# Optimization experiments

Measured on AMD Instinct MI355X. Metric: run time of the kernel, lower is better.

## Reference

```python
import jax, jax.numpy as jnp
import numpy as np

N = 20000      # nodes
E = 160000     # edges
IN = 32        # in_dim == hidden_dim
H = 32         # hidden_dim
EF = 95        # edge_feat_dim
EH = 64        # edge_hidden
G = 64         # graphs in batch
EPS = 1e-5     # BatchNorm eps


def setup_inputs() -> dict:
    key = jax.random.key(0)
    ks = jax.random.split(key, 40)
    d = {}
    d["x"] = jax.random.normal(ks[0], (N, IN), dtype=jnp.float32)
    d["edge_src"] = jax.random.randint(ks[1], (E,), 0, N)
    d["edge_dst"] = jax.random.randint(ks[2], (E,), 0, N)
    d["edge_attr"] = jax.random.normal(ks[3], (E, EF), dtype=jnp.float32)
    d["batch"] = jnp.sort(jax.random.randint(ks[4], (N,), 0, G))
    k = 5
    for i, c_in in enumerate([IN, H]):
        c_out = H
        d[f"conv{i}_W1"] = jax.random.normal(ks[k], (EF, EH)) * 0.1; k += 1
        d[f"conv{i}_b1"] = jnp.zeros((EH,), jnp.float32)
        d[f"conv{i}_W2"] = jax.random.normal(ks[k], (EH, c_in * c_out)) * 0.02; k += 1
        d[f"conv{i}_b2"] = jnp.zeros((c_in * c_out,), jnp.float32)
        d[f"conv{i}_root"] = jax.random.normal(ks[k], (c_in, c_out)) * 0.1; k += 1
        d[f"conv{i}_bias"] = jnp.zeros((c_out,), jnp.float32)
        d[f"bn{i}_g"] = jnp.ones((c_out,), jnp.float32)
        d[f"bn{i}_b"] = jnp.zeros((c_out,), jnp.float32)
        d[f"bn{i}_rm"] = jnp.zeros((c_out,), jnp.float32)
        d[f"bn{i}_rv"] = jnp.ones((c_out,), jnp.float32)
    d["lin1_W"] = jax.random.normal(ks[k], (H, H)) * 0.1; k += 1
    d["lin1_b"] = jnp.zeros((H,), jnp.float32)
    d["lin2_W"] = jax.random.normal(ks[k], (H, 2)) * 0.1; k += 1
    d["lin2_b"] = jnp.zeros((2,), jnp.float32)
    return d


def _nnconv(x, src, dst, e, W1, b1, W2, b2, root, bias, c_in, c_out):
    # edge MLP -> per-edge weight matrix Theta: [E, c_in, c_out]
    h = jax.nn.relu(e @ W1 + b1)
    theta = (h @ W2 + b2).reshape(-1, c_in, c_out)
    # message: x_src (gather) times per-edge matrix, scatter-add to dst
    msg = jnp.einsum('ei,eio->eo', x[src], theta)
    agg = jax.ops.segment_sum(msg, dst, num_segments=N)
    return agg + x @ root + bias


def _bn_eval(x, g, b, rm, rv):
    return (x - rm) * jax.lax.rsqrt(rv + EPS) * g + b


def reference(x, edge_src, edge_dst, edge_attr, batch,
              conv0_W1, conv0_b1, conv0_W2, conv0_b2, conv0_root, conv0_bias,
              bn0_g, bn0_b, bn0_rm, bn0_rv,
              conv1_W1, conv1_b1, conv1_W2, conv1_b2, conv1_root, conv1_bias,
              bn1_g, bn1_b, bn1_rm, bn1_rv,
              lin1_W, lin1_b, lin2_W, lin2_b):
    x = _nnconv(x, edge_src, edge_dst, edge_attr,
                conv0_W1, conv0_b1, conv0_W2, conv0_b2, conv0_root, conv0_bias, IN, H)
    x = jax.nn.relu(_bn_eval(x, bn0_g, bn0_b, bn0_rm, bn0_rv))
    x = _nnconv(x, edge_src, edge_dst, edge_attr,
                conv1_W1, conv1_b1, conv1_W2, conv1_b2, conv1_root, conv1_bias, H, H)
    x = jax.nn.relu(_bn_eval(x, bn1_g, bn1_b, bn1_rm, bn1_rv))
    # global max pool over graphs
    g = jax.ops.segment_max(x, batch, num_segments=G)
    g = jax.nn.relu(g @ lin1_W + lin1_b)
    return g @ lin2_W + lin2_b
```

## Files before the change

kernel.cpp:

```cpp
#include <hip/hip_runtime.h>

#define NN   20000
#define NE   160000
#define HD   32
#define EFD  95
#define EHD  64
#define NG   64
#define EPSF 1e-5f

__global__ __launch_bounds__(256) void zero_kernel(float* __restrict__ p, int n) {
    int i = blockIdx.x * 256 + threadIdx.x;
    if (i < n) p[i] = 0.f;
}

__global__ __launch_bounds__(256) void hist_kernel(const int* __restrict__ idx,
                                                   int* __restrict__ hist) {
    const int e = blockIdx.x * 256 + threadIdx.x;
    atomicAdd(&hist[idx[e]], 1);
}

__global__ __launch_bounds__(1024) void scan_kernel(const int* __restrict__ hist,
                                                    int* __restrict__ rowptr,
                                                    int* __restrict__ cursor) {
    __shared__ int part[1024];
    const int t = threadIdx.x;
    const int base = t * 20;
    int s = 0;
    #pragma unroll
    for (int k = 0; k < 20; ++k) {
        const int idx = base + k;
        if (idx < NN) s += hist[idx];
    }
    part[t] = s;
    __syncthreads();
    for (int off = 1; off < 1024; off <<= 1) {
        int v = 0;
        if (t >= off) v = part[t - off];
        __syncthreads();
        if (t >= off) part[t] += v;
        __syncthreads();
    }
    int run = part[t] - s;
    #pragma unroll
    for (int k = 0; k < 20; ++k) {
        const int idx = base + k;
        if (idx < NN) {
            rowptr[idx] = run;
            cursor[idx] = run;
            run += hist[idx];
        }
    }
    if (t == 0) rowptr[NN] = NE;
}

__global__ __launch_bounds__(256) void scatter_dst_kernel(const int* __restrict__ dst,
                                                          int* __restrict__ cursor,
                                                          int* __restrict__ sortpos) {
    const int e = blockIdx.x * 256 + threadIdx.x;
    sortpos[e] = atomicAdd(&cursor[dst[e]], 1);
}

__global__ __launch_bounds__(256) void scatter_src_kernel(const int* __restrict__ src,
                                                          const int* __restrict__ sortpos_d,
                                                          int* __restrict__ cursor,
                                                          int* __restrict__ ssorted,
                                                          int* __restrict__ wpos,
                                                          int* __restrict__ esorted) {
    const int e = blockIdx.x * 256 + threadIdx.x;
    const int s = src[e];
    const int pos = atomicAdd(&cursor[s], 1);
    ssorted[pos] = s;
    wpos[pos]    = sortpos_d[e];
    esorted[pos] = e;
}

__global__ __launch_bounds__(256) void edge_mlp_kernel(
    const float* __restrict__ ea, const float* __restrict__ W1,
    const float* __restrict__ b1, float* __restrict__ hT)
{
    __shared__ float elds[128 * EFD];
    const int tid = threadIdx.x;
    const int e0  = blockIdx.x * 128;
    const float4* s4 = reinterpret_cast<const float4*>(ea + (size_t)e0 * EFD);
    float4* d4 = reinterpret_cast<float4*>(elds);
    #pragma unroll
    for (int i = 0; i < 12; ++i) {
        const int idx = tid + i * 256;
        if (idx < (128 * EFD / 4)) d4[idx] = s4[idx];
    }
    __syncthreads();
    const int el = tid & 127;
    const int hh = (tid >> 7) * 32;
    const int e  = e0 + el;
    float acc[32];
    #pragma unroll
    for (int k = 0; k < 32; ++k) acc[k] = b1[hh + k];
    const float* er = elds + el * EFD;
    #pragma unroll 5
    for (int j = 0; j < EFD; ++j) {
        const float ej = er[j];
        const float* w1r = W1 + j * EHD + hh;
        #pragma unroll
        for (int k = 0; k < 32; ++k)
            acc[k] = fmaf(ej, w1r[k], acc[k]);
    }
    #pragma unroll
    for (int k = 0; k < 32; ++k)
        hT[(hh + k) * NE + e] = fmaxf(acc[k], 0.f);
}

__global__ __launch_bounds__(256) void edge_mlp_v7_kernel(
    const float* __restrict__ ea,
    const float* __restrict__ W1,
    const float* __restrict__ b1,
    float*       __restrict__ hs)
{
    __shared__ float alds[64 * 100];
    __shared__ float wlds[96 * 64];
    const int tid = threadIdx.x;
    const int e0  = blockIdx.x * 64;

    {
        const float4* s4 = reinterpret_cast<const float4*>(ea + (size_t)e0 * EFD);
        #pragma unroll
        for (int it = 0; it < 6; ++it) {
            const int idx4 = tid + it * 256;
            if (idx4 < (64 * EFD / 4)) {
                const float4 v = s4[idx4];
                const unsigned f = (unsigned)idx4 * 4u;
                const float vv[4] = {v.x, v.y, v.z, v.w};
                #pragma unroll
                for (int t = 0; t < 4; ++t) {
                    const unsigned ft = f + t;
                    const unsigned et = (ft * 44151u) >> 22;
                    const unsigned jt = ft - 95u * et;
                    alds[et * 100 + jt] = vv[t];
                }
            }
        }
    }
    {
        const float4* w4 = reinterpret_cast<const float4*>(W1);
        float4* d4 = reinterpret_cast<float4*>(wlds);
        #pragma unroll
        for (int it = 0; it < 6; ++it) {
            const int idx4 = tid + it * 256;
            if (idx4 < (EFD * EHD / 4)) d4[idx4] = w4[idx4];
        }
    }
    if (tid < 64) {
        alds[tid * 100 + 95] = 0.f;
        wlds[95 * 64 + tid]  = 0.f;
    }
    __syncthreads();

    const int tx = tid & 15;
    const int ty = tid >> 4;

    float acc[4][4];
    {
        const float4 bv4 = *reinterpret_cast<const float4*>(b1 + 4 * tx);
        const float bb[4] = {bv4.x, bv4.y, bv4.z, bv4.w};
        #pragma unroll
        for (int i = 0; i < 4; ++i)
            #pragma unroll
            for (int c = 0; c < 4; ++c)
                acc[i][c] = bb[c];
    }

    for (int jq = 0; jq < 24; ++jq) {
        float w[4][4];
        #pragma unroll
        for (int r = 0; r < 4; ++r) {
            const float4 wv = *reinterpret_cast<const float4*>(
                &wlds[(4 * jq + r) * 64 + 4 * tx]);
            w[r][0] = wv.x; w[r][1] = wv.y; w[r][2] = wv.z; w[r][3] = wv.w;
        }
        #pragma unroll
        for (int i = 0; i < 4; ++i) {
            const float4 av = *reinterpret_cast<const float4*>(
                &alds[(4 * ty + i) * 100 + 4 * jq]);
            #pragma unroll
            for (int c = 0; c < 4; ++c) {
                float t0 = fmaf(av.x, w[0][c], acc[i][c]);
                t0 = fmaf(av.y, w[1][c], t0);
                t0 = fmaf(av.z, w[2][c], t0);
                acc[i][c] = fmaf(av.w, w[3][c], t0);
            }
        }
    }

    #pragma unroll
    for (int i = 0; i < 4; ++i) {
        const int e = e0 + 4 * ty + i;
        float4 v;
        v.x = fmaxf(acc[i][0], 0.f);
        v.y = fmaxf(acc[i][1], 0.f);
        v.z = fmaxf(acc[i][2], 0.f);
        v.w = fmaxf(acc[i][3], 0.f);
        *reinterpret_cast<float4*>(hs + (size_t)e * EHD + 4 * tx) = v;
    }
}

__global__ __launch_bounds__(256) void tmat_kernel(
    const float* __restrict__ xin,
    const float* __restrict__ W2,
    float*       __restrict__ T)
{
    const int nb = blockIdx.x * 8;
    const int c  = blockIdx.y * 256 + threadIdx.x;
    const int kh = c >> 5, o = c & 31;

    float w[32];
    const float* wp = W2 + kh * 1024 + o;
    #pragma unroll
    for (int i = 0; i < 32; ++i) w[i] = wp[i * 32];

    #pragma unroll
    for (int nj = 0; nj < 8; ++nj) {
        const float* xr = xin + (nb + nj) * HD;
        float a0 = 0.f, a1 = 0.f;
        #pragma unroll
        for (int i = 0; i < 32; i += 2) {
            a0 = fmaf(xr[i],     w[i],     a0);
            a1 = fmaf(xr[i + 1], w[i + 1], a1);
        }
        T[(size_t)(nb + nj) * 2048 + c] = a0 + a1;
    }
}

__global__ __launch_bounds__(256) void bvec_kernel(
    const float* __restrict__ xin, const float* __restrict__ b2,
    float* __restrict__ bv)
{
    const int gid = blockIdx.x * 256 + threadIdx.x;
    const int n = gid >> 5, o = gid & 31;
    const float* xr = xin + n * HD;
    float a = 0.f;
    #pragma unroll
    for (int i = 0; i < 32; ++i)
        a = fmaf(xr[i], b2[i * HD + o], a);
    bv[gid] = a;
}

__global__ __launch_bounds__(256) void emsg_kernel(
    const int*   __restrict__ ssorted, const int* __restrict__ wpos,
    const int*   __restrict__ esorted,
    const float* __restrict__ hs,
    const float* __restrict__ T,
    const float* __restrict__ bv,
    float*       __restrict__ msg)
{
    __shared__ float hl[8 * EHD];
    const int tid = threadIdx.x;
    const int p0  = blockIdx.x * 8;

    if (tid < 128) {
        const int q   = tid >> 4;
        const int eid = esorted[p0 + q];
        reinterpret_cast<float4*>(hl)[tid] =
            reinterpret_cast<const float4*>(hs + (size_t)eid * EHD)[tid & 15];
    }
    __syncthreads();

    const int sl = tid >> 5, o = tid & 31;
    const int p  = p0 + sl;
    const int s  = ssorted[p];
    const int wp = wpos[p];

    float hreg[EHD];
    #pragma unroll
    for (int q = 0; q < 16; ++q) {
        const float4 v = reinterpret_cast<const float4*>(hl + sl * EHD)[q];
        hreg[q * 4] = v.x; hreg[q * 4 + 1] = v.y;
        hreg[q * 4 + 2] = v.z; hreg[q * 4 + 3] = v.w;
    }

    const float* tr = T + (size_t)s * 2048 + o;
    float a0 = bv[s * HD + o], a1 = 0.f;
    #pragma unroll
    for (int kh = 0; kh < EHD; kh += 2) {
        a0 = fmaf(hreg[kh],     tr[kh * 32],       a0);
        a1 = fmaf(hreg[kh + 1], tr[(kh + 1) * 32], a1);
    }
    msg[(size_t)wp * HD + o] = a0 + a1;
}

__global__ __launch_bounds__(64) void nnconv_kernel(
    const float* __restrict__ xin, const int* __restrict__ src,
    const int* __restrict__ sortpos, const float* __restrict__ hT,
    const float* __restrict__ W2, const float* __restrict__ b2,
    float* __restrict__ msg)
{
    const int e  = blockIdx.x * 64 + threadIdx.x;
    const int oh = blockIdx.y * 16;
    const int s  = src[e];
    const int sp = sortpos[e];
    float xs[HD];
    {
        const float* xr = xin + s * HD;
        #pragma unroll
        for (int i = 0; i < HD; i += 4) {
            const float4 v = *reinterpret_cast<const float4*>(xr + i);
            xs[i] = v.x; xs[i + 1] = v.y; xs[i + 2] = v.z; xs[i + 3] = v.w;
        }
    }
    float acc[16];
    #pragma unroll
    for (int o = 0; o < 16; ++o) acc[o] = 0.f;
    #pragma unroll 1
    for (int kh = 0; kh < EHD; ++kh) {
        const float hk = hT[kh * NE + e];
        const float* w2k = W2 + kh * (HD * HD) + oh;
        #pragma unroll
        for (int i = 0; i < HD; ++i) {
            const float p = hk * xs[i];
            #pragma unroll
            for (int o = 0; o < 16; ++o)
                acc[o] = fmaf(p, w2k[i * HD + o], acc[o]);
        }
    }
    #pragma unroll 1
    for (int i = 0; i < HD; ++i) {
        const float xi = xs[i];
        const float* b2r = b2 + i * HD + oh;
        #pragma unroll
        for (int o = 0; o < 16; ++o)
            acc[o] = fmaf(xi, b2r[o], acc[o]);
    }
    float* mr = msg + sp * HD + oh;
    #pragma unroll
    for (int q = 0; q < 4; ++q) {
        float4 v;
        v.x = acc[q * 4 + 0]; v.y = acc[q * 4 + 1];
        v.z = acc[q * 4 + 2]; v.w = acc[q * 4 + 3];
        *reinterpret_cast<float4*>(mr + q * 4) = v;
    }
}

__global__ __launch_bounds__(256) void node_update_kernel(
    const int*   __restrict__ rowptr, const float* __restrict__ msg,
    const float* __restrict__ xin,
    const float* __restrict__ root, const float* __restrict__ bias,
    const float* __restrict__ bg, const float* __restrict__ bb,
    const float* __restrict__ brm, const float* __restrict__ brv,
    float* __restrict__ xout)
{
    const int gid = blockIdx.x * 256 + threadIdx.x;
    const int n = gid >> 5, o = gid & 31;
    float a = 0.f;
    const int j0 = rowptr[n], j1 = rowptr[n + 1];
    for (int j = j0; j < j1; ++j)
        a += msg[j * HD + o];
    const float* xr = xin + n * HD;
    #pragma unroll
    for (int i = 0; i < HD; ++i)
        a = fmaf(xr[i], root[i * HD + o], a);
    a += bias[o];
    a = (a - brm[o]) * rsqrtf(brv[o] + EPSF) * bg[o] + bb[o];
    xout[gid] = fmaxf(a, 0.f);
}

__global__ __launch_bounds__(256) void node_update_pool_kernel(
    const int*   __restrict__ rowptr, const float* __restrict__ msg,
    const float* __restrict__ xin, const int* __restrict__ batch,
    const float* __restrict__ root, const float* __restrict__ bias,
    const float* __restrict__ bg, const float* __restrict__ bb,
    const float* __restrict__ brm, const float* __restrict__ brv,
    float* __restrict__ g)
{
    const int gid = blockIdx.x * 256 + threadIdx.x;
    const int n = gid >> 5, o = gid & 31;
    float a = 0.f;
    const int j0 = rowptr[n], j1 = rowptr[n + 1];
    for (int j = j0; j < j1; ++j)
        a += msg[j * HD + o];
    const float* xr = xin + n * HD;
    #pragma unroll
    for (int i = 0; i < HD; ++i)
        a = fmaf(xr[i], root[i * HD + o], a);
    a += bias[o];
    a = (a - brm[o]) * rsqrtf(brv[o] + EPSF) * bg[o] + bb[o];
    a = fmaxf(a, 0.f);
    atomicMax(reinterpret_cast<int*>(g) + batch[n] * HD + o, __float_as_int(a));
}

__global__ __launch_bounds__(256) void pool_kernel(
    const float* __restrict__ x, const int* __restrict__ batch,
    float* __restrict__ g)
{
    const int gid = blockIdx.x * 256 + threadIdx.x;
    const int n = gid >> 5, o = gid & 31;
    const float v = x[gid];
    atomicMax(reinterpret_cast<int*>(g) + batch[n] * HD + o, __float_as_int(v));
}

__global__ __launch_bounds__(64) void head_kernel(
    const float* __restrict__ g, const float* __restrict__ l1W,
    const float* __restrict__ l1b, const float* __restrict__ l2W,
    const float* __restrict__ l2b, float* __restrict__ out)
{
    const int gr = threadIdx.x;
    const float* grow = g + gr * HD;
    float hv[HD];
    #pragma unroll
    for (int o = 0; o < HD; ++o) hv[o] = l1b[o];
    #pragma unroll
    for (int i = 0; i < HD; ++i) {
        const float gi = grow[i];
        #pragma unroll
        for (int o = 0; o < HD; ++o)
            hv[o] = fmaf(gi, l1W[i * HD + o], hv[o]);
    }
    float o0 = l2b[0], o1 = l2b[1];
    #pragma unroll
    for (int o = 0; o < HD; ++o) {
        const float r = fmaxf(hv[o], 0.f);
        o0 = fmaf(r, l2W[o * 2 + 0], o0);
        o1 = fmaf(r, l2W[o * 2 + 1], o1);
    }
    out[gr * 2 + 0] = o0;
    out[gr * 2 + 1] = o1;
}

extern "C" void kernel_launch(void* const* d_in, const int* in_sizes, int n_in,
                              void* d_out, int out_size, void* d_ws, size_t ws_size,
                              hipStream_t stream)
{
    const float* x     = (const float*)d_in[0];
    const int*   esrc  = (const int*)  d_in[1];
    const int*   edst  = (const int*)  d_in[2];
    const float* eattr = (const float*)d_in[3];
    const int*   batch = (const int*)  d_in[4];

    const float* c0W1   = (const float*)d_in[5];
    const float* c0b1   = (const float*)d_in[6];
    const float* c0W2   = (const float*)d_in[7];
    const float* c0b2   = (const float*)d_in[8];
    const float* c0root = (const float*)d_in[9];
    const float* c0bias = (const float*)d_in[10];
    const float* bn0g   = (const float*)d_in[11];
    const float* bn0b   = (const float*)d_in[12];
    const float* bn0rm  = (const float*)d_in[13];
    const float* bn0rv  = (const float*)d_in[14];

    const float* c1W1   = (const float*)d_in[15];
    const float* c1b1   = (const float*)d_in[16];
    const float* c1W2   = (const float*)d_in[17];
    const float* c1b2   = (const float*)d_in[18];
    const float* c1root = (const float*)d_in[19];
    const float* c1bias = (const float*)d_in[20];
    const float* bn1g   = (const float*)d_in[21];
    const float* bn1b   = (const float*)d_in[22];
    const float* bn1rm  = (const float*)d_in[23];
    const float* bn1rv  = (const float*)d_in[24];

    const float* l1W = (const float*)d_in[25];
    const float* l1b = (const float*)d_in[26];
    const float* l2W = (const float*)d_in[27];
    const float* l2b = (const float*)d_in[28];

    float* ws   = (float*)d_ws;
    float* hbuf = ws;
    float* msg  = ws + 10240000;
    float* x1   = ws + 15360000;
    float* x2   = ws + 16000000;
    float* gbuf = ws + 16640000;
    int* hist_d    = (int*)(ws + 16642048);
    int* hist_s    = (int*)(ws + 16662048);
    int* rowptr_d  = (int*)(ws + 16682048);
    int* cursor_d  = (int*)(ws + 16702049);
    int* sortpos_d = (int*)(ws + 16722049);
    int* rowptr_s  = (int*)(ws + 16882049);
    int* cursor_s  = (int*)(ws + 16902050);
    int* ssorted   = (int*)(ws + 16922050);
    int* wpos      = (int*)(ws + 17082050);
    int* esorted   = (int*)(ws + 17242050);
    float* bv      = ws + 17402050;
    float* T       = ws + 18042050;
    const size_t NEED_NEW = (size_t)59002050 * 4;
    const bool use_fast = (ws_size >= NEED_NEW);

    zero_kernel<<<165, 256, 0, stream>>>(gbuf, 42048);

    hist_kernel<<<NE / 256, 256, 0, stream>>>(edst, hist_d);
    scan_kernel<<<1, 1024, 0, stream>>>(hist_d, rowptr_d, cursor_d);
    scatter_dst_kernel<<<NE / 256, 256, 0, stream>>>(edst, cursor_d, sortpos_d);

    if (use_fast) {
        hist_kernel<<<NE / 256, 256, 0, stream>>>(esrc, hist_s);
        scan_kernel<<<1, 1024, 0, stream>>>(hist_s, rowptr_s, cursor_s);
        scatter_src_kernel<<<NE / 256, 256, 0, stream>>>(esrc, sortpos_d, cursor_s,
                                                         ssorted, wpos, esorted);
        const dim3 tgrid(NN / 8, 8);
        bvec_kernel<<<NN * HD / 256, 256, 0, stream>>>(x, c0b2, bv);
        tmat_kernel<<<tgrid, 256, 0, stream>>>(x, c0W2, T);
        edge_mlp_v7_kernel<<<NE / 64, 256, 0, stream>>>(eattr, c0W1, c0b1, hbuf);
        emsg_kernel<<<NE / 8, 256, 0, stream>>>(ssorted, wpos, esorted, hbuf, T, bv, msg);
        node_update_kernel<<<NN * HD / 256, 256, 0, stream>>>(rowptr_d, msg, x, c0root, c0bias,
                                                              bn0g, bn0b, bn0rm, bn0rv, x1);
        bvec_kernel<<<NN * HD / 256, 256, 0, stream>>>(x1, c1b2, bv);
        tmat_kernel<<<tgrid, 256, 0, stream>>>(x1, c1W2, T);
        edge_mlp_v7_kernel<<<NE / 64, 256, 0, stream>>>(eattr, c1W1, c1b1, hbuf);
        emsg_kernel<<<NE / 8, 256, 0, stream>>>(ssorted, wpos, esorted, hbuf, T, bv, msg);
        node_update_pool_kernel<<<NN * HD / 256, 256, 0, stream>>>(rowptr_d, msg, x1, batch,
                                                                   c1root, c1bias,
                                                                   bn1g, bn1b, bn1rm, bn1rv, gbuf);
    } else {
        const dim3 egrid64(NE / 64, 2);
        edge_mlp_kernel<<<NE / 128, 256, 0, stream>>>(eattr, c0W1, c0b1, hbuf);
        nnconv_kernel<<<egrid64, 64, 0, stream>>>(x, esrc, sortpos_d, hbuf, c0W2, c0b2, msg);
        node_update_kernel<<<NN * HD / 256, 256, 0, stream>>>(rowptr_d, msg, x, c0root, c0bias,
                                                              bn0g, bn0b, bn0rm, bn0rv, x1);
        edge_mlp_kernel<<<NE / 128, 256, 0, stream>>>(eattr, c1W1, c1b1, hbuf);
        nnconv_kernel<<<egrid64, 64, 0, stream>>>(x1, esrc, sortpos_d, hbuf, c1W2, c1b2, msg);
        node_update_kernel<<<NN * HD / 256, 256, 0, stream>>>(rowptr_d, msg, x1, c1root, c1bias,
                                                              bn1g, bn1b, bn1rm, bn1rv, x2);
        pool_kernel<<<NN * HD / 256, 256, 0, stream>>>(x2, batch, gbuf);
    }

    head_kernel<<<1, 64, 0, stream>>>(gbuf, l1W, l1b, l2W, l2b, (float*)d_out);
}
```

Measured before the change: 643.8 us.

## Fuse per-node T matrix computation into message kernel via shared memory

```diff
diff --git a/kernel.cpp b/kernel.cpp
--- a/kernel.cpp
+++ b/kernel.cpp
@@ -7,6 +7,7 @@
 #define EHD  64
 #define NG   64
 #define EPSF 1e-5f
+#define NPB  4
 
 __global__ __launch_bounds__(256) void zero_kernel(float* __restrict__ p, int n) {
     int i = blockIdx.x * 256 + threadIdx.x;
@@ -202,33 +203,6 @@
     }
 }
 
-__global__ __launch_bounds__(256) void tmat_kernel(
-    const float* __restrict__ xin,
-    const float* __restrict__ W2,
-    float*       __restrict__ T)
-{
-    const int nb = blockIdx.x * 8;
-    const int c  = blockIdx.y * 256 + threadIdx.x;
-    const int kh = c >> 5, o = c & 31;
-
-    float w[32];
-    const float* wp = W2 + kh * 1024 + o;
-    #pragma unroll
-    for (int i = 0; i < 32; ++i) w[i] = wp[i * 32];
-
-    #pragma unroll
-    for (int nj = 0; nj < 8; ++nj) {
-        const float* xr = xin + (nb + nj) * HD;
-        float a0 = 0.f, a1 = 0.f;
-        #pragma unroll
-        for (int i = 0; i < 32; i += 2) {
-            a0 = fmaf(xr[i],     w[i],     a0);
-            a1 = fmaf(xr[i + 1], w[i + 1], a1);
-        }
-        T[(size_t)(nb + nj) * 2048 + c] = a0 + a1;
-    }
-}
-
 __global__ __launch_bounds__(256) void bvec_kernel(
     const float* __restrict__ xin, const float* __restrict__ b2,
     float* __restrict__ bv)
@@ -243,47 +217,75 @@
     bv[gid] = a;
 }
 
-__global__ __launch_bounds__(256) void emsg_kernel(
-    const int*   __restrict__ ssorted, const int* __restrict__ wpos,
+__global__ __launch_bounds__(256) void tmsg_kernel(
+    const float* __restrict__ xin,
+    const float* __restrict__ W2,
+    const int*   __restrict__ rowptr_s,
+    const int*   __restrict__ ssorted,
+    const int*   __restrict__ wpos,
     const int*   __restrict__ esorted,
     const float* __restrict__ hs,
-    const float* __restrict__ T,
     const float* __restrict__ bv,
     float*       __restrict__ msg)
 {
+    __shared__ float Tl[NPB * 2048];
     __shared__ float hl[8 * EHD];
     const int tid = threadIdx.x;
-    const int p0  = blockIdx.x * 8;
-
-    if (tid < 128) {
-        const int q   = tid >> 4;
-        const int eid = esorted[p0 + q];
-        reinterpret_cast<float4*>(hl)[tid] =
-            reinterpret_cast<const float4*>(hs + (size_t)eid * EHD)[tid & 15];
+    const int n0  = blockIdx.x * NPB;
+
+    #pragma unroll 1
+    for (int cg = 0; cg < 8; ++cg) {
+        const int c  = cg * 256 + tid;
+        const int kh = c >> 5, o = c & 31;
+        float w[32];
+        const float* wp = W2 + kh * 1024 + o;
+        #pragma unroll
+        for (int i = 0; i < 32; ++i) w[i] = wp[i * 32];
+        #pragma unroll
+        for (int n = 0; n < NPB; ++n) {
+            const float* xr = xin + (size_t)(n0 + n) * HD;
+            float a0 = 0.f, a1 = 0.f;
+            #pragma unroll
+            for (int i = 0; i < 32; i += 2) {
+                a0 = fmaf(xr[i],     w[i],     a0);
+                a1 = fmaf(xr[i + 1], w[i + 1], a1);
+            }
+            Tl[n * 2048 + c] = a0 + a1;
+        }
     }
     __syncthreads();
 
+    const int p_begin = rowptr_s[n0];
+    const int p_end   = rowptr_s[n0 + NPB];
     const int sl = tid >> 5, o = tid & 31;
-    const int p  = p0 + sl;
-    const int s  = ssorted[p];
-    const int wp = wpos[p];
-
-    float hreg[EHD];
-    #pragma unroll
-    for (int q = 0; q < 16; ++q) {
-        const float4 v = reinterpret_cast<const float4*>(hl + sl * EHD)[q];
-        hreg[q * 4] = v.x; hreg[q * 4 + 1] = v.y;
-        hreg[q * 4 + 2] = v.z; hreg[q * 4 + 3] = v.w;
-    }
-
-    const float* tr = T + (size_t)s * 2048 + o;
-    float a0 = bv[s * HD + o], a1 = 0.f;
-    #pragma unroll
-    for (int kh = 0; kh < EHD; kh += 2) {
-        a0 = fmaf(hreg[kh],     tr[kh * 32],       a0);
-        a1 = fmaf(hreg[kh + 1], tr[(kh + 1) * 32], a1);
-    }
-    msg[(size_t)wp * HD + o] = a0 + a1;
+
+    #pragma unroll 1
+    for (int pb = p_begin; pb < p_end; pb += 8) {
+        const int nrows = min(8, p_end - pb);
+        if (tid < nrows * 16) {
+            const int q   = tid >> 4;
+            const int eid = esorted[pb + q];
+            reinterpret_cast<float4*>(hl)[tid] =
+                reinterpret_cast<const float4*>(hs + (size_t)eid * EHD)[tid & 15];
+        }
+        __syncthreads();
+
+        if (sl < nrows) {
+            const int p  = pb + sl;
+            const int s  = ssorted[p];
+            const int wp = wpos[p];
+            const float* hr = hl + sl * EHD;
+            const float* tr = Tl + (s - n0) * 2048 + o;
+            float a0 = bv[s * HD + o], a1 = 0.f;
+            #pragma unroll
+            for (int kh = 0; kh < EHD; kh += 2) {
+                a0 = fmaf(hr[kh],     tr[kh * 32],       a0);
+                a1 = fmaf(hr[kh + 1], tr[(kh + 1) * 32], a1);
+            }
+            msg[(size_t)wp * HD + o] = a0 + a1;
+        }
+        __syncthreads();
+    }
 }
 
 __global__ __launch_bounds__(64) void nnconv_kernel(
@@ -477,8 +479,7 @@
     int* wpos      = (int*)(ws + 17082050);
     int* esorted   = (int*)(ws + 17242050);
     float* bv      = ws + 17402050;
-    float* T       = ws + 18042050;
-    const size_t NEED_NEW = (size_t)59002050 * 4;
+    const size_t NEED_NEW = (size_t)18042050 * 4;
     const bool use_fast = (ws_size >= NEED_NEW);
 
     zero_kernel<<<165, 256, 0, stream>>>(gbuf, 42048);
@@ -492,17 +493,16 @@
         scan_kernel<<<1, 1024, 0, stream>>>(hist_s, rowptr_s, cursor_s);
         scatter_src_kernel<<<NE / 256, 256, 0, stream>>>(esrc, sortpos_d, cursor_s,
                                                          ssorted, wpos, esorted);
-        const dim3 tgrid(NN / 8, 8);
         bvec_kernel<<<NN * HD / 256, 256, 0, stream>>>(x, c0b2, bv);
-        tmat_kernel<<<tgrid, 256, 0, stream>>>(x, c0W2, T);
         edge_mlp_v7_kernel<<<NE / 64, 256, 0, stream>>>(eattr, c0W1, c0b1, hbuf);
-        emsg_kernel<<<NE / 8, 256, 0, stream>>>(ssorted, wpos, esorted, hbuf, T, bv, msg);
+        tmsg_kernel<<<NN / NPB, 256, 0, stream>>>(x, c0W2, rowptr_s, ssorted, wpos,
+                                                  esorted, hbuf, bv, msg);
         node_update_kernel<<<NN * HD / 256, 256, 0, stream>>>(rowptr_d, msg, x, c0root, c0bias,
                                                               bn0g, bn0b, bn0rm, bn0rv, x1);
         bvec_kernel<<<NN * HD / 256, 256, 0, stream>>>(x1, c1b2, bv);
-        tmat_kernel<<<tgrid, 256, 0, stream>>>(x1, c1W2, T);
         edge_mlp_v7_kernel<<<NE / 64, 256, 0, stream>>>(eattr, c1W1, c1b1, hbuf);
-        emsg_kernel<<<NE / 8, 256, 0, stream>>>(ssorted, wpos, esorted, hbuf, T, bv, msg);
+        tmsg_kernel<<<NN / NPB, 256, 0, stream>>>(x1, c1W2, rowptr_s, ssorted, wpos,
+                                                  esorted, hbuf, bv, msg);
         node_update_pool_kernel<<<NN * HD / 256, 256, 0, stream>>>(rowptr_d, msg, x1, batch,
                                                                    c1root, c1bias,
                                                                    bn1g, bn1b, bn1rm, bn1rv, gbuf);
```

New measurement: 607.0 us. -5.7%, faster.
